# Kernel tuning notes

Hardware: AMD Instinct MI355X
Metric: run time of the kernel (lower is better)

Reference implementation:

```python
import jax, jax.numpy as jnp
import numpy as np

BS, Q, NC, T, NI = 16, 1000, 80, 100, 8
IMG_W, IMG_H = 1333.0, 800.0
ALPHA, GAMMA = 0.25, 2.0
W_CLASS, W_BBOX, W_GIOU = 2.0, 5.0, 2.0


def _rand_boxes(key, n):
    k1, k2 = jax.random.split(key)
    cxcy = jax.random.uniform(k1, (n, 2)) * jnp.array([IMG_W, IMG_H])
    wh = jax.random.uniform(k2, (n, 2)) * 300.0 + 8.0
    return jnp.concatenate([cxcy - wh / 2, cxcy + wh / 2], axis=-1).astype(jnp.float32)


def setup_inputs() -> dict:
    key = jax.random.key(0)
    k1, k2, k3, k4, k5 = jax.random.split(key, 5)
    img_sz = jnp.array([IMG_W, IMG_H, IMG_W, IMG_H], jnp.float32)
    return {
        'pred_logits': jax.random.normal(k1, (BS, Q, NC), jnp.float32),
        'pred_boxes': _rand_boxes(k2, BS * Q).reshape(BS, Q, 4),
        'tgt_bbox': _rand_boxes(k3, BS * T),
        'ign_bbox': _rand_boxes(k4, BS * NI),
        'image_size_xyxy': jnp.tile(img_sz, (BS, 1)),
        'image_size_xyxy_tgt': jnp.tile(img_sz, (BS * T, 1)),
        'tgt_ids': jax.random.randint(k5, (BS * T,), 0, NC),
    }


def _area(b):
    return (b[:, 2] - b[:, 0]) * (b[:, 3] - b[:, 1])


def _pairwise_inter(b1, b2):
    # b1: [N,4], b2: [M,4] -> inter area [N,M]
    lt = jnp.maximum(b1[:, None, :2], b2[None, :, :2])
    rb = jnp.minimum(b1[:, None, 2:], b2[None, :, 2:])
    wh = jnp.clip(rb - lt, 0.0)
    return wh[..., 0] * wh[..., 1]


def _giou(b1, b2):
    inter = _pairwise_inter(b1, b2)
    union = _area(b1)[:, None] + _area(b2)[None, :] - inter
    iou = inter / union
    # smallest enclosing box
    lt = jnp.minimum(b1[:, None, :2], b2[None, :, :2])
    rb = jnp.maximum(b1[:, None, 2:], b2[None, :, 2:])
    wh = jnp.clip(rb - lt, 0.0)
    enc = wh[..., 0] * wh[..., 1]
    return iou - (enc - union) / enc


def reference(pred_logits, pred_boxes, tgt_bbox, ign_bbox, image_size_xyxy,
              image_size_xyxy_tgt, tgt_ids):
    bs, q, nc = pred_logits.shape
    n = bs * q
    out_prob = jax.nn.sigmoid(pred_logits.reshape(n, nc))          # focal branch
    out_bbox = pred_boxes.reshape(n, 4)

    # focal classification cost, gathered at target labels
    p = out_prob[:, tgt_ids]                                       # [N, T_total]
    neg = (1 - ALPHA) * p ** GAMMA * (-jnp.log(1 - p + 1e-8))
    pos = ALPHA * (1 - p) ** GAMMA * (-jnp.log(p + 1e-8))
    cost_class = pos - neg

    # L1 cost on normalized boxes
    img_out = jnp.repeat(image_size_xyxy, q, axis=0)               # [N,4]
    ob = out_bbox / img_out
    tb = tgt_bbox / image_size_xyxy_tgt
    cost_bbox = jnp.abs(ob[:, None, :] - tb[None, :, :]).sum(-1)   # [N, T_total]

    cost_giou = -_giou(out_bbox, tgt_bbox)

    # IoA of predictions vs ignore boxes (intersection / pred area)
    ioa = _pairwise_inter(out_bbox, ign_bbox) / _area(out_bbox)[:, None]

    C = W_BBOX * cost_bbox + W_CLASS * cost_class + W_GIOU * cost_giou

    # per-image block-diagonal extraction (homogeneous T, NI per image)
    t = tgt_bbox.shape[0] // bs
    ni = ign_bbox.shape[0] // bs
    idx = jnp.arange(bs)
    C_diag = C.reshape(bs, q, bs, t)[idx, :, idx, :]               # [bs, Q, T]
    ioa_diag = ioa.reshape(bs, q, bs, ni)[idx, :, idx, :]          # [bs, Q, NI]
    return C_diag, ioa_diag
```

## Files before the change

### kernel.cpp

```cpp
#include <hip/hip_runtime.h>

constexpr int BS = 16, Q = 1000, NC = 80, T = 100, NI = 8;
constexpr int CTOT = BS * Q * T;
constexpr int ITOT = BS * Q * NI;
constexpr int TOT  = CTOT + ITOT;

#define ALPHA   0.25f
#define W_CLASS 2.0f
#define W_BBOX  5.0f
#define W_GIOU  2.0f

__device__ __forceinline__ float rcp(float x)  { return __builtin_amdgcn_rcpf(x); }
__device__ __forceinline__ float ex2(float x)  { return __builtin_amdgcn_exp2f(x); }
__device__ __forceinline__ float lg2(float x)  { return __builtin_amdgcn_logf(x); }
#define LOG2E 1.44269504088896f
#define LN2   0.69314718055995f

__global__ __launch_bounds__(256) void matcher_kernel(
    const float* __restrict__ pred_logits,
    const float* __restrict__ pred_boxes,
    const float* __restrict__ tgt_bbox,
    const float* __restrict__ ign_bbox,
    const float* __restrict__ img_sz,
    const float* __restrict__ img_sz_tgt,
    const int*   __restrict__ tgt_ids,
    float* __restrict__ out)
{
    const int idx = blockIdx.x * 256 + threadIdx.x;
    if (idx >= TOT) return;

    if (idx < CTOT) {
        const int n = idx / T;
        const int j = idx - n * T;
        const int b = n / Q;
        const int r = b * T + j;

        const float4 pb  = *(const float4*)(pred_boxes  + (size_t)n * 4);
        const float4 tb  = *(const float4*)(tgt_bbox    + (size_t)r * 4);
        const float4 isz = *(const float4*)(img_sz      + (size_t)b * 4);
        const float4 tsz = *(const float4*)(img_sz_tgt  + (size_t)r * 4);

        const float cb = fabsf(pb.x * rcp(isz.x) - tb.x * rcp(tsz.x))
                       + fabsf(pb.y * rcp(isz.y) - tb.y * rcp(tsz.y))
                       + fabsf(pb.z * rcp(isz.z) - tb.z * rcp(tsz.z))
                       + fabsf(pb.w * rcp(isz.w) - tb.w * rcp(tsz.w));

        const int   cls   = tgt_ids[r];
        const float logit = pred_logits[(size_t)n * NC + cls];
        const float p     = rcp(1.0f + ex2(-logit * LOG2E));
        const float omp   = 1.0f - p;
        const float pos   =  ALPHA         * omp * omp * (-(lg2(p   + 1e-8f) * LN2));
        const float neg   = (1.0f - ALPHA) * p   * p   * (-(lg2(omp + 1e-8f) * LN2));
        const float cost_class = pos - neg;

        const float area_p = (pb.z - pb.x) * (pb.w - pb.y);
        const float area_t = (tb.z - tb.x) * (tb.w - tb.y);
        const float iw  = fmaxf(fminf(pb.z, tb.z) - fmaxf(pb.x, tb.x), 0.0f);
        const float ih  = fmaxf(fminf(pb.w, tb.w) - fmaxf(pb.y, tb.y), 0.0f);
        const float inter = iw * ih;
        const float uni   = area_p + area_t - inter;
        const float ew  = fmaxf(fmaxf(pb.z, tb.z) - fminf(pb.x, tb.x), 0.0f);
        const float eh  = fmaxf(fmaxf(pb.w, tb.w) - fminf(pb.y, tb.y), 0.0f);
        const float enc = ew * eh;
        const float giou = inter * rcp(uni) - (enc - uni) * rcp(enc);

        out[idx] = W_BBOX * cb + W_CLASS * cost_class - W_GIOU * giou;
    } else {
        const int k = idx - CTOT;
        const int n = k >> 3;
        const int j = k & (NI - 1);
        const int b = n / Q;
        const int r = b * NI + j;

        const float4 pb = *(const float4*)(pred_boxes + (size_t)n * 4);
        const float4 ib = *(const float4*)(ign_bbox   + (size_t)r * 4);
        const float area_p = (pb.z - pb.x) * (pb.w - pb.y);
        const float iw  = fmaxf(fminf(pb.z, ib.z) - fmaxf(pb.x, ib.x), 0.0f);
        const float ih  = fmaxf(fminf(pb.w, ib.w) - fmaxf(pb.y, ib.y), 0.0f);
        out[idx] = iw * ih * rcp(area_p);
    }
}

extern "C" void kernel_launch(void* const* d_in, const int* in_sizes, int n_in,
                              void* d_out, int out_size, void* d_ws, size_t ws_size,
                              hipStream_t stream) {
    const float* pred_logits = (const float*)d_in[0];
    const float* pred_boxes  = (const float*)d_in[1];
    const float* tgt_bbox    = (const float*)d_in[2];
    const float* ign_bbox    = (const float*)d_in[3];
    const float* img_sz      = (const float*)d_in[4];
    const float* img_sz_tgt  = (const float*)d_in[5];
    const int*   tgt_ids     = (const int*)d_in[6];
    float* out = (float*)d_out;

    const int blocks = (TOT + 255) / 256;
    matcher_kernel<<<blocks, 256, 0, stream>>>(
        pred_logits, pred_boxes, tgt_bbox, ign_bbox, img_sz, img_sz_tgt, tgt_ids, out);
}
```

Baseline: 72.71 us.

## Split box normalization into a pre-pass and compute four targets per thread

A small pre-kernel normalizes prediction and target boxes into the workspace, which removes the per-element reciprocal divisions. The main kernel has each thread compute four consecutive target costs, or all eight ignore IoA values, sharing the prediction box and writing float4 stores. The focal cost is rewritten so one exp2 and one log2 serve both terms, which drops the 1e-8 epsilon. GIoU now runs on normalized boxes, which is only equivalent when prediction and target scales match per axis. The extra kernel launch and workspace round trip are added costs.

```diff
diff --git a/kernel.cpp b/kernel.cpp
--- a/kernel.cpp
+++ b/kernel.cpp
@@ -1,83 +1,115 @@
 #include <hip/hip_runtime.h>
 
 constexpr int BS = 16, Q = 1000, NC = 80, T = 100, NI = 8;
-constexpr int CTOT = BS * Q * T;
-constexpr int ITOT = BS * Q * NI;
-constexpr int TOT  = CTOT + ITOT;
+constexpr int NP   = BS * Q;
+constexpr int NR   = BS * T;
+constexpr int CTOT = NP * T;
+constexpr int ITOT = NP * NI;
+constexpr int C4   = CTOT / 4;
+constexpr int MAIN = C4 + NP;
 
 #define ALPHA   0.25f
 #define W_CLASS 2.0f
 #define W_BBOX  5.0f
 #define W_GIOU  2.0f
+#define LOG2E 1.44269504088896f
+#define LN2   0.69314718055995f
 
 __device__ __forceinline__ float rcp(float x)  { return __builtin_amdgcn_rcpf(x); }
 __device__ __forceinline__ float ex2(float x)  { return __builtin_amdgcn_exp2f(x); }
 __device__ __forceinline__ float lg2(float x)  { return __builtin_amdgcn_logf(x); }
-#define LOG2E 1.44269504088896f
-#define LN2   0.69314718055995f
 
-__global__ __launch_bounds__(256) void matcher_kernel(
+__global__ __launch_bounds__(256) void pre_norm(
+    const float* __restrict__ pred_boxes,
+    const float* __restrict__ tgt_bbox,
+    const float* __restrict__ img_sz,
+    const float* __restrict__ img_sz_tgt,
+    float4* __restrict__ ws)
+{
+    const int t = blockIdx.x * 256 + threadIdx.x;
+    if (t < NP) {
+        const int b = t / Q;
+        const float4 pb = *((const float4*)pred_boxes + t);
+        const float4 s  = *((const float4*)img_sz + b);
+        ws[t] = make_float4(pb.x * rcp(s.x), pb.y * rcp(s.y),
+                            pb.z * rcp(s.z), pb.w * rcp(s.w));
+    } else if (t < NP + NR) {
+        const int r = t - NP;
+        const float4 tb = *((const float4*)tgt_bbox + r);
+        const float4 s  = *((const float4*)img_sz_tgt + r);
+        ws[NP + r] = make_float4(tb.x * rcp(s.x), tb.y * rcp(s.y),
+                                 tb.z * rcp(s.z), tb.w * rcp(s.w));
+    }
+}
+
+__global__ __launch_bounds__(256) void matcher_main(
     const float* __restrict__ pred_logits,
     const float* __restrict__ pred_boxes,
-    const float* __restrict__ tgt_bbox,
     const float* __restrict__ ign_bbox,
-    const float* __restrict__ img_sz,
-    const float* __restrict__ img_sz_tgt,
     const int*   __restrict__ tgt_ids,
+    const float4* __restrict__ ws,
     float* __restrict__ out)
 {
     const int idx = blockIdx.x * 256 + threadIdx.x;
-    if (idx >= TOT) return;
+    if (idx < C4) {
+        const int n  = idx / 25;
+        const int jg = (idx - n * 25) << 2;
+        const int b  = n / Q;
+        const int r0 = b * T + jg;
 
-    if (idx < CTOT) {
-        const int n = idx / T;
-        const int j = idx - n * T;
+        const float4 pbn = ws[n];
+        const float area_p = (pbn.z - pbn.x) * (pbn.w - pbn.y);
+
+        const int4 cls4 = *(const int4*)(tgt_ids + r0);
+        const float* lgp = pred_logits + (size_t)n * NC;
+
+        float c[4];
+        #pragma unroll
+        for (int k = 0; k < 4; ++k) {
+            const float4 tbn = ws[NP + r0 + k];
+            const int   cls = (&cls4.x)[k];
+            const float x   = lgp[cls];
+
+            const float cb = fabsf(pbn.x - tbn.x) + fabsf(pbn.y - tbn.y)
+                           + fabsf(pbn.z - tbn.z) + fabsf(pbn.w - tbn.w);
+
+            const float e   = ex2(-x * LOG2E);
+            const float p   = rcp(1.0f + e);
+            const float omp = e * p;
+            const float L   = lg2(1.0f + e) * LN2;
+            const float cc  = ALPHA * omp * omp * L
+                            - (1.0f - ALPHA) * p * p * (x + L);
+
+            const float area_t = (tbn.z - tbn.x) * (tbn.w - tbn.y);
+            const float iw  = fminf(pbn.z, tbn.z) - fmaxf(pbn.x, tbn.x);
+            const float ih  = fminf(pbn.w, tbn.w) - fmaxf(pbn.y, tbn.y);
+            const float inter = fmaxf(iw, 0.0f) * fmaxf(ih, 0.0f);
+            const float uni   = area_p + area_t - inter;
+            const float ew  = fmaxf(pbn.z, tbn.z) - fminf(pbn.x, tbn.x);
+            const float eh  = fmaxf(pbn.w, tbn.w) - fminf(pbn.y, tbn.y);
+            const float enc = ew * eh;
+            const float giou = inter * rcp(uni) - (enc - uni) * rcp(enc);
+
+            c[k] = W_BBOX * cb + W_CLASS * cc - W_GIOU * giou;
+        }
+        *(float4*)(out + (size_t)n * T + jg) = make_float4(c[0], c[1], c[2], c[3]);
+    } else {
+        const int n = idx - C4;
         const int b = n / Q;
-        const int r = b * T + j;
-
-        const float4 pb  = *(const float4*)(pred_boxes  + (size_t)n * 4);
-        const float4 tb  = *(const float4*)(tgt_bbox    + (size_t)r * 4);
-        const float4 isz = *(const float4*)(img_sz      + (size_t)b * 4);
-        const float4 tsz = *(const float4*)(img_sz_tgt  + (size_t)r * 4);
-
-        const float cb = fabsf(pb.x * rcp(isz.x) - tb.x * rcp(tsz.x))
-                       + fabsf(pb.y * rcp(isz.y) - tb.y * rcp(tsz.y))
-                       + fabsf(pb.z * rcp(isz.z) - tb.z * rcp(tsz.z))
-                       + fabsf(pb.w * rcp(isz.w) - tb.w * rcp(tsz.w));
-
-        const int   cls   = tgt_ids[r];
-        const float logit = pred_logits[(size_t)n * NC + cls];
-        const float p     = rcp(1.0f + ex2(-logit * LOG2E));
-        const float omp   = 1.0f - p;
-        const float pos   =  ALPHA         * omp * omp * (-(lg2(p   + 1e-8f) * LN2));
-        const float neg   = (1.0f - ALPHA) * p   * p   * (-(lg2(omp + 1e-8f) * LN2));
-        const float cost_class = pos - neg;
-
-        const float area_p = (pb.z - pb.x) * (pb.w - pb.y);
-        const float area_t = (tb.z - tb.x) * (tb.w - tb.y);
-        const float iw  = fmaxf(fminf(pb.z, tb.z) - fmaxf(pb.x, tb.x), 0.0f);
-        const float ih  = fmaxf(fminf(pb.w, tb.w) - fmaxf(pb.y, tb.y), 0.0f);
-        const float inter = iw * ih;
-        const float uni   = area_p + area_t - inter;
-        const float ew  = fmaxf(fmaxf(pb.z, tb.z) - fminf(pb.x, tb.x), 0.0f);
-        const float eh  = fmaxf(fmaxf(pb.w, tb.w) - fminf(pb.y, tb.y), 0.0f);
-        const float enc = ew * eh;
-        const float giou = inter * rcp(uni) - (enc - uni) * rcp(enc);
-
-        out[idx] = W_BBOX * cb + W_CLASS * cost_class - W_GIOU * giou;
-    } else {
-        const int k = idx - CTOT;
-        const int n = k >> 3;
-        const int j = k & (NI - 1);
-        const int b = n / Q;
-        const int r = b * NI + j;
-
-        const float4 pb = *(const float4*)(pred_boxes + (size_t)n * 4);
-        const float4 ib = *(const float4*)(ign_bbox   + (size_t)r * 4);
-        const float area_p = (pb.z - pb.x) * (pb.w - pb.y);
-        const float iw  = fmaxf(fminf(pb.z, ib.z) - fmaxf(pb.x, ib.x), 0.0f);
-        const float ih  = fmaxf(fminf(pb.w, ib.w) - fmaxf(pb.y, ib.y), 0.0f);
-        out[idx] = iw * ih * rcp(area_p);
+        const float4 pb = *((const float4*)pred_boxes + n);
+        const float ra  = rcp((pb.z - pb.x) * (pb.w - pb.y));
+        const float4* ib = (const float4*)ign_bbox + b * NI;
+        float o[8];
+        #pragma unroll
+        for (int k = 0; k < 8; ++k) {
+            const float4 g = ib[k];
+            const float iw = fmaxf(fminf(pb.z, g.z) - fmaxf(pb.x, g.x), 0.0f);
+            const float ih = fmaxf(fminf(pb.w, g.w) - fmaxf(pb.y, g.y), 0.0f);
+            o[k] = iw * ih * ra;
+        }
+        float4* dst = (float4*)(out + CTOT + (size_t)n * NI);
+        dst[0] = make_float4(o[0], o[1], o[2], o[3]);
+        dst[1] = make_float4(o[4], o[5], o[6], o[7]);
     }
 }
 
@@ -93,7 +125,9 @@
     const int*   tgt_ids     = (const int*)d_in[6];
     float* out = (float*)d_out;
 
-    const int blocks = (TOT + 255) / 256;
-    matcher_kernel<<<blocks, 256, 0, stream>>>(
-        pred_logits, pred_boxes, tgt_bbox, ign_bbox, img_sz, img_sz_tgt, tgt_ids, out);
+    pre_norm<<<(NP + NR + 255) / 256, 256, 0, stream>>>(
+        pred_boxes, tgt_bbox, img_sz, img_sz_tgt, (float4*)d_ws);
+
+    matcher_main<<<MAIN / 256, 256, 0, stream>>>(
+        pred_logits, pred_boxes, ign_bbox, tgt_ids, (const float4*)d_ws, out);
 }
```

Result: no change. 73.47 us (+1.0%).
